# Performance work log

Measured on AMD Instinct MI355X. Metric: run time of the kernel, lower is better.

The kernel has to match this reference:

```python
import jax, jax.numpy as jnp
import numpy as np

DIM = 256
HID = 128


def setup_inputs() -> dict:
    key = jax.random.key(0)
    ks = jax.random.split(key, 10)
    B, T = 8, 2048
    s_in = 1.0 / np.sqrt(DIM)
    s_h = 1.0 / np.sqrt(HID)
    return {
        "x": jax.random.normal(ks[0], (B, T, DIM), jnp.float32),
        "adapt_bias": jax.random.normal(ks[1], (B, T, T), jnp.float32),
        "Wq": jax.random.uniform(ks[2], (HID, DIM), jnp.float32, -s_in, s_in),
        "bq": jax.random.uniform(ks[3], (HID,), jnp.float32, -s_in, s_in),
        "Wk": jax.random.uniform(ks[4], (HID, DIM), jnp.float32, -s_in, s_in),
        "bk": jax.random.uniform(ks[5], (HID,), jnp.float32, -s_in, s_in),
        "Wv": jax.random.uniform(ks[6], (HID, DIM), jnp.float32, -s_in, s_in),
        "bv": jax.random.uniform(ks[7], (HID,), jnp.float32, -s_in, s_in),
        "Wp": jax.random.uniform(ks[8], (DIM, HID), jnp.float32, -s_h, s_h),
        "bp": jax.random.uniform(ks[9], (DIM,), jnp.float32, -s_h, s_h),
    }


def reference(x, adapt_bias, Wq, bq, Wk, bk, Wv, bv, Wp, bp):
    # y = x (default). Q,K,V: [B,T,H]
    Q = jnp.einsum('btd,hd->bth', x, Wq) + bq
    K = jnp.einsum('btd,hd->bth', x, Wk) + bk
    V = jnp.einsum('btd,hd->bth', x, Wv) + bv
    Q_sig = jax.nn.sigmoid(Q)
    ab = jax.nn.softmax(adapt_bias, axis=-1)        # [B,T,T]
    Ksm = jax.nn.softmax(K, axis=1)                 # softmax over time dim
    eab = jnp.exp(ab)                               # [B,T,T]
    eK = jnp.exp(Ksm)                               # [B,T,H]
    num = jnp.einsum('bts,bsh->bth', eab, eK * V)
    den = jnp.einsum('bts,bsh->bth', eab, eK)
    Yt = Q_sig * (num / den)                        # [B,T,H]
    return jnp.einsum('bth,dh->btd', Yt, Wp) + bp   # [B,T,DIM]
```

## Files before the change

### kernel.cpp

```cpp
#include <hip/hip_runtime.h>
#include <hip/hip_bf16.h>

#define B_ 8
#define T_ 2048
#define D_ 256
#define H_ 128

typedef float f32x4 __attribute__((ext_vector_type(4)));
typedef short bf16x8 __attribute__((ext_vector_type(8)));

__device__ __forceinline__ unsigned short f2bf(float f){
  union { float f; unsigned u; } v; v.f = f;
  unsigned u = v.u;
  unsigned r = (u + 0x7FFFu + ((u >> 16) & 1u)) >> 16;
  return (unsigned short)r;
}

#define GLL16(g, l) __builtin_amdgcn_global_load_lds( \
    (const __attribute__((address_space(1))) void*)(g), \
    (__attribute__((address_space(3))) void*)(l), 16, 0, 0)

__device__ __forceinline__ float blk_reduce(float v, bool is_max, float* sbuf){
  for(int o = 32; o > 0; o >>= 1){
    float t = __shfl_xor(v, o);
    v = is_max ? fmaxf(v, t) : (v + t);
  }
  int w = threadIdx.x >> 6;
  __syncthreads();
  if((threadIdx.x & 63) == 0) sbuf[w] = v;
  __syncthreads();
  float r = sbuf[0];
  for(int i = 1; i < 4; i++) r = is_max ? fmaxf(r, sbuf[i]) : (r + sbuf[i]);
  return r;
}

__global__ __launch_bounds__(256) void qkv_kernel(
    const float* __restrict__ x,
    const float* __restrict__ Wq, const float* __restrict__ bq,
    const float* __restrict__ Wk, const float* __restrict__ bk,
    const float* __restrict__ Wv, const float* __restrict__ bv,
    float* __restrict__ Qsig, float* __restrict__ Kt, float* __restrict__ Vt)
{
  const int mat = blockIdx.y;
  const int g0  = blockIdx.x * 64;
  const int tid = threadIdx.x;
  const float* W   = (mat == 0) ? Wq : (mat == 1) ? Wk : Wv;
  const float* bia = (mat == 0) ? bq : (mat == 1) ? bk : bv;

  __shared__ __align__(16) short As[64 * 32];
  __shared__ __align__(16) short Ws[128 * 32];
  __shared__ float tbuf[64][129];

  const int w = tid >> 6, lane = tid & 63, rl = lane & 15, kg = lane >> 4;
  f32x4 acc[8];
  for(int i = 0; i < 8; i++) acc[i] = (f32x4){0.f, 0.f, 0.f, 0.f};

  const int c = tid & 31, r8 = tid >> 5;
  for(int kk = 0; kk < 256; kk += 32){
    __syncthreads();
    for(int p = 0; p < 8; p++){
      int rr = r8 + p * 8;
      As[rr * 32 + c] = (short)f2bf(x[(size_t)(g0 + rr) * 256 + kk + c]);
    }
    for(int p = 0; p < 16; p++){
      int hh = r8 + p * 8;
      Ws[hh * 32 + c] = (short)f2bf(W[(size_t)hh * 256 + kk + c]);
    }
    __syncthreads();
    bf16x8 a = *(const bf16x8*)&As[(w * 16 + rl) * 32 + kg * 8];
    for(int cf = 0; cf < 8; cf++){
      bf16x8 bb = *(const bf16x8*)&Ws[(cf * 16 + rl) * 32 + kg * 8];
      acc[cf] = __builtin_amdgcn_mfma_f32_16x16x32_bf16(a, bb, acc[cf], 0, 0, 0);
    }
  }

  const int b = g0 >> 11, t0 = g0 & 2047;
  if(mat == 0){
    for(int cf = 0; cf < 8; cf++){
      int h = cf * 16 + rl;
      float bh = bia[h];
      for(int r = 0; r < 4; r++){
        int tl = w * 16 + kg * 4 + r;
        float v = acc[cf][r] + bh;
        Qsig[(size_t)(g0 + tl) * 128 + h] = 1.f / (1.f + __expf(-v));
      }
    }
  } else {
    for(int cf = 0; cf < 8; cf++){
      int h = cf * 16 + rl;
      float bh = bia[h];
      for(int r = 0; r < 4; r++){
        int tl = w * 16 + kg * 4 + r;
        tbuf[tl][h] = acc[cf][r] + bh;
      }
    }
    __syncthreads();
    float* dst = (mat == 1) ? Kt : Vt;
    int h = tid >> 1, part = tid & 1;
    float* drow = dst + (size_t)(b * 128 + h) * 2048 + t0 + part * 32;
    for(int i = 0; i < 32; i += 4){
      float4 o;
      o.x = tbuf[part * 32 + i + 0][h];
      o.y = tbuf[part * 32 + i + 1][h];
      o.z = tbuf[part * 32 + i + 2][h];
      o.w = tbuf[part * 32 + i + 3][h];
      *(float4*)(drow + i) = o;
    }
  }
}

__global__ __launch_bounds__(256) void colsm_kernel(
    const float* __restrict__ Kt, const float* __restrict__ Vt,
    unsigned short* __restrict__ Mt)
{
  __shared__ float sbuf[4];
  const int b  = blockIdx.x >> 5;
  const int hg = blockIdx.x & 31;
  const int tid = threadIdx.x;
  for(int i = 0; i < 4; i++){
    int h = hg * 4 + i;
    const float* kr = Kt + (size_t)(b * 128 + h) * 2048;
    const float* vr = Vt + (size_t)(b * 128 + h) * 2048;
    float4 k0 = *(const float4*)(kr + tid * 4);
    float4 k1 = *(const float4*)(kr + tid * 4 + 1024);
    float m = fmaxf(fmaxf(fmaxf(k0.x, k0.y), fmaxf(k0.z, k0.w)),
                    fmaxf(fmaxf(k1.x, k1.y), fmaxf(k1.z, k1.w)));
    m = blk_reduce(m, true, sbuf);
    float s = __expf(k0.x - m) + __expf(k0.y - m) + __expf(k0.z - m) + __expf(k0.w - m)
            + __expf(k1.x - m) + __expf(k1.y - m) + __expf(k1.z - m) + __expf(k1.w - m);
    s = blk_reduce(s, false, sbuf);
    float iz = 1.f / s;
    float4 v0 = *(const float4*)(vr + tid * 4);
    float4 v1 = *(const float4*)(vr + tid * 4 + 1024);
    unsigned short* ekvp = Mt + (size_t)(b * 256 + h) * 2048;
    unsigned short* ekp  = Mt + (size_t)(b * 256 + 128 + h) * 2048;
    ushort4 pv, pe;
    float e;
    e = __expf(__expf(k0.x - m) * iz); pv.x = f2bf(e * v0.x); pe.x = f2bf(e);
    e = __expf(__expf(k0.y - m) * iz); pv.y = f2bf(e * v0.y); pe.y = f2bf(e);
    e = __expf(__expf(k0.z - m) * iz); pv.z = f2bf(e * v0.z); pe.z = f2bf(e);
    e = __expf(__expf(k0.w - m) * iz); pv.w = f2bf(e * v0.w); pe.w = f2bf(e);
    ((ushort4*)ekvp)[tid] = pv;
    ((ushort4*)ekp)[tid]  = pe;
    e = __expf(__expf(k1.x - m) * iz); pv.x = f2bf(e * v1.x); pe.x = f2bf(e);
    e = __expf(__expf(k1.y - m) * iz); pv.y = f2bf(e * v1.y); pe.y = f2bf(e);
    e = __expf(__expf(k1.z - m) * iz); pv.z = f2bf(e * v1.z); pe.z = f2bf(e);
    e = __expf(__expf(k1.w - m) * iz); pv.w = f2bf(e * v1.w); pe.w = f2bf(e);
    ((ushort4*)ekvp)[tid + 256] = pv;
    ((ushort4*)ekp)[tid + 256]  = pe;
  }
}

__global__ __launch_bounds__(256) void softexp_kernel(
    const float* __restrict__ ab, unsigned short* __restrict__ eab)
{
  __shared__ float sbuf[4];
  const size_t row = blockIdx.x;
  const float* r = ab + row * 2048;
  const int tid = threadIdx.x;
  float4 v0 = *(const float4*)(r + tid * 4);
  float4 v1 = *(const float4*)(r + tid * 4 + 1024);
  float m = fmaxf(fmaxf(fmaxf(v0.x, v0.y), fmaxf(v0.z, v0.w)),
                  fmaxf(fmaxf(v1.x, v1.y), fmaxf(v1.z, v1.w)));
  m = blk_reduce(m, true, sbuf);
  float e0x = __expf(v0.x - m), e0y = __expf(v0.y - m);
  float e0z = __expf(v0.z - m), e0w = __expf(v0.w - m);
  float e1x = __expf(v1.x - m), e1y = __expf(v1.y - m);
  float e1z = __expf(v1.z - m), e1w = __expf(v1.w - m);
  float s = e0x + e0y + e0z + e0w + e1x + e1y + e1z + e1w;
  s = blk_reduce(s, false, sbuf);
  float iz = 1.f / s;
  ushort4 o;
  o.x = f2bf(__expf(e0x * iz)); o.y = f2bf(__expf(e0y * iz));
  o.z = f2bf(__expf(e0z * iz)); o.w = f2bf(__expf(e0w * iz));
  *(ushort4*)(eab + row * 2048 + tid * 4) = o;
  o.x = f2bf(__expf(e1x * iz)); o.y = f2bf(__expf(e1y * iz));
  o.z = f2bf(__expf(e1z * iz)); o.w = f2bf(__expf(e1w * iz));
  *(ushort4*)(eab + row * 2048 + tid * 4 + 1024) = o;
}

__global__ __launch_bounds__(256) void aft_gemm4(
    const unsigned short* __restrict__ eab,
    const unsigned short* __restrict__ Mt,
    const float* __restrict__ Qsig,
    unsigned short* __restrict__ Yt)
{
  __shared__ __align__(16) unsigned short As2[2][64 * 64];
  __shared__ __align__(16) unsigned short Bs2[2][128 * 64];

  const int bid = blockIdx.x;
  const int b   = bid & 7;
  const int idx = bid >> 3;
  const int rt  = idx >> 1;
  const int hb  = idx & 1;
  const int t0  = rt * 64;
  const int h0  = hb * 64;

  const int tid = threadIdx.x;
  const int w = tid >> 6, lane = tid & 63;
  const int rl = lane & 15, kg = lane >> 4;
  const int wr = w >> 1, wc = w & 1;

  const int lr = lane >> 3;
  const int cc = (lane & 7) ^ lr;

  const size_t rowbase = (size_t)b * 2048 + t0;
  const unsigned short* a_src = eab + (rowbase + (size_t)(w * 16 + lr)) * 2048 + cc * 8;
  const int mtrow = (w < 2) ? (h0 + w * 32 + lr) : (128 + h0 + (w - 2) * 32 + lr);
  const unsigned short* b_src = Mt + ((size_t)b * 256 + mtrow) * 2048 + cc * 8;

  f32x4 acc[2][4];
#pragma unroll
  for(int i = 0; i < 2; i++)
#pragma unroll
    for(int j = 0; j < 4; j++) acc[i][j] = (f32x4){0.f, 0.f, 0.f, 0.f};

  auto stage = [&](int buf, int t){
#pragma unroll
    for(int i = 0; i < 2; i++)
      GLL16(a_src + (size_t)i * 8 * 2048 + t * 64, &As2[buf][(w * 16 + i * 8) * 64]);
#pragma unroll
    for(int i = 0; i < 4; i++)
      GLL16(b_src + (size_t)i * 8 * 2048 + t * 64, &Bs2[buf][(w * 32 + i * 8) * 64]);
  };

  const int rx = rl & 7;
  stage(0, 0);
  stage(1, 1);

  for(int t = 0; t < 32; ++t){
    const int cur = t & 1;
    if(t < 31) asm volatile("s_waitcnt vmcnt(6)" ::: "memory");
    else       asm volatile("s_waitcnt vmcnt(0)" ::: "memory");
    __builtin_amdgcn_s_barrier();
    asm volatile("" ::: "memory");

    bf16x8 af[2][2], bf[2][4];
#pragma unroll
    for(int ks = 0; ks < 2; ++ks){
      const int slot = ((ks * 4 + kg) ^ rx) * 8;
      af[ks][0] = *(const bf16x8*)&As2[cur][(wr * 32 + rl) * 64 + slot];
      af[ks][1] = *(const bf16x8*)&As2[cur][(wr * 32 + 16 + rl) * 64 + slot];
#pragma unroll
      for(int cf = 0; cf < 4; ++cf){
        const int brow = ((cf < 2) ? (wc * 32 + cf * 16)
                                   : (64 + wc * 32 + (cf - 2) * 16)) + rl;
        bf[ks][cf] = *(const bf16x8*)&Bs2[cur][brow * 64 + slot];
      }
    }
    asm volatile("s_waitcnt lgkmcnt(0)" ::: "memory");
    __builtin_amdgcn_sched_barrier(0);
    __builtin_amdgcn_s_barrier();
    asm volatile("" ::: "memory");

    if(t < 30) stage(cur, t + 2);

    __builtin_amdgcn_s_setprio(1);
#pragma unroll
    for(int ks = 0; ks < 2; ++ks)
#pragma unroll
      for(int cf = 0; cf < 4; ++cf){
        acc[0][cf] = __builtin_amdgcn_mfma_f32_16x16x32_bf16(af[ks][0], bf[ks][cf], acc[0][cf], 0, 0, 0);
        acc[1][cf] = __builtin_amdgcn_mfma_f32_16x16x32_bf16(af[ks][1], bf[ks][cf], acc[1][cf], 0, 0, 0);
      }
    __builtin_amdgcn_s_setprio(0);
  }

#pragma unroll
  for(int rf = 0; rf < 2; ++rf)
#pragma unroll
    for(int cf = 0; cf < 2; ++cf){
      const int h = h0 + wc * 32 + cf * 16 + rl;
#pragma unroll
      for(int r = 0; r < 4; ++r){
        const int tl = wr * 32 + rf * 16 + kg * 4 + r;
        const size_t g = rowbase + tl;
        float num = acc[rf][cf][r], den = acc[rf][cf + 2][r];
        float q = Qsig[g * 128 + h];
        Yt[g * 128 + h] = f2bf(q * num / den);
      }
    }
}

__global__ __launch_bounds__(256) void outproj_kernel(
    const unsigned short* __restrict__ Yt, const float* __restrict__ Wp,
    const float* __restrict__ bp, float* __restrict__ out)
{
  __shared__ __align__(16) short As[64 * 32];
  __shared__ __align__(16) short Bs[256 * 32];
  const int g0 = blockIdx.x * 64;
  const int tid = threadIdx.x;
  const int w = tid >> 6, lane = tid & 63, rl = lane & 15, kg = lane >> 4;
  f32x4 acc[16];
  for(int i = 0; i < 16; i++) acc[i] = (f32x4){0.f, 0.f, 0.f, 0.f};

  const int ar = tid >> 2, apart = tid & 3;
  const int c = tid & 31, dr = tid >> 5;
  for(int k = 0; k < 128; k += 32){
    __syncthreads();
    *(uint4*)&As[ar * 32 + apart * 8] =
        *(const uint4*)(Yt + (size_t)(g0 + ar) * 128 + k + apart * 8);
    for(int p = 0; p < 32; p++){
      int d = dr + p * 8;
      Bs[d * 32 + c] = (short)f2bf(Wp[(size_t)d * 128 + k + c]);
    }
    __syncthreads();
    bf16x8 a = *(const bf16x8*)&As[(w * 16 + rl) * 32 + kg * 8];
    for(int cf = 0; cf < 16; cf++){
      bf16x8 bb = *(const bf16x8*)&Bs[(cf * 16 + rl) * 32 + kg * 8];
      acc[cf] = __builtin_amdgcn_mfma_f32_16x16x32_bf16(a, bb, acc[cf], 0, 0, 0);
    }
  }
  for(int cf = 0; cf < 16; cf++){
    int d = cf * 16 + rl;
    float bpd = bp[d];
    for(int r = 0; r < 4; r++){
      int tl = w * 16 + kg * 4 + r;
      out[(size_t)(g0 + tl) * 256 + d] = acc[cf][r] + bpd;
    }
  }
}

extern "C" void kernel_launch(void* const* d_in, const int* in_sizes, int n_in,
                              void* d_out, int out_size, void* d_ws, size_t ws_size,
                              hipStream_t stream)
{
  const float* x  = (const float*)d_in[0];
  const float* ab = (const float*)d_in[1];
  const float* Wq = (const float*)d_in[2];
  const float* bq = (const float*)d_in[3];
  const float* Wk = (const float*)d_in[4];
  const float* bk = (const float*)d_in[5];
  const float* Wv = (const float*)d_in[6];
  const float* bv = (const float*)d_in[7];
  const float* Wp = (const float*)d_in[8];
  const float* bp = (const float*)d_in[9];
  float* out = (float*)d_out;

  char* ws = (char*)d_ws;
  float* Qsig          = (float*)(ws);
  float* Kt            = (float*)(ws + 8388608);
  float* Vt            = (float*)(ws + 16777216);
  unsigned short* Mt   = (unsigned short*)(ws + 25165824);
  unsigned short* eab  = (unsigned short*)(ws + 33554432);
  unsigned short* Yt   = (unsigned short*)(ws + 8388608);

  qkv_kernel<<<dim3(256, 3), 256, 0, stream>>>(x, Wq, bq, Wk, bk, Wv, bv, Qsig, Kt, Vt);
  colsm_kernel<<<256, 256, 0, stream>>>(Kt, Vt, Mt);
  softexp_kernel<<<16384, 256, 0, stream>>>(ab, eab);
  aft_gemm4<<<512, 256, 0, stream>>>(eab, Mt, Qsig, Yt);
  outproj_kernel<<<256, 256, 0, stream>>>(Yt, Wp, bp, out);
}
```

Baseline: 96.51 us.

## Enlarge AFT GEMM tile to 128 rows with triple-buffered LDS, single barrier

The main AFT GEMM block tile grows from 64 to 128 time rows, so each loaded Mt tile is reused across twice as many rows and the grid halves to 256 blocks. The LDS pipeline moves from double to triple buffering, which drops the second barrier per k-step, issues the prefetch right after the first barrier, and interleaves LDS reads with MFMAs. The cost is more LDS and accumulator registers per block and fewer blocks, which may lower occupancy and leave some of the 256 CUs with less overlap.

```diff
diff --git a/kernel.cpp b/kernel.cpp
--- a/kernel.cpp
+++ b/kernel.cpp
@@ -179,21 +179,21 @@
   *(ushort4*)(eab + row * 2048 + tid * 4 + 1024) = o;
 }
 
-__global__ __launch_bounds__(256) void aft_gemm4(
+__global__ __launch_bounds__(256) void aft_gemm5(
     const unsigned short* __restrict__ eab,
     const unsigned short* __restrict__ Mt,
     const float* __restrict__ Qsig,
     unsigned short* __restrict__ Yt)
 {
-  __shared__ __align__(16) unsigned short As2[2][64 * 64];
-  __shared__ __align__(16) unsigned short Bs2[2][128 * 64];
+  __shared__ __align__(16) unsigned short As2[3][128 * 64];
+  __shared__ __align__(16) unsigned short Bs2[3][128 * 64];
 
   const int bid = blockIdx.x;
   const int b   = bid & 7;
   const int idx = bid >> 3;
   const int rt  = idx >> 1;
   const int hb  = idx & 1;
-  const int t0  = rt * 64;
+  const int t0  = rt * 128;
   const int h0  = hb * 64;
 
   const int tid = threadIdx.x;
@@ -201,24 +201,24 @@
   const int rl = lane & 15, kg = lane >> 4;
   const int wr = w >> 1, wc = w & 1;
 
-  const int lr = lane >> 3;
-  const int cc = (lane & 7) ^ lr;
+  const int lr8 = lane >> 3;
+  const int cc  = (lane & 7) ^ lr8;
 
   const size_t rowbase = (size_t)b * 2048 + t0;
-  const unsigned short* a_src = eab + (rowbase + (size_t)(w * 16 + lr)) * 2048 + cc * 8;
-  const int mtrow = (w < 2) ? (h0 + w * 32 + lr) : (128 + h0 + (w - 2) * 32 + lr);
+  const unsigned short* a_src = eab + (rowbase + (size_t)(w * 32 + lr8)) * 2048 + cc * 8;
+  const int mtrow = (w < 2) ? (h0 + w * 32 + lr8) : (128 + h0 + (w - 2) * 32 + lr8);
   const unsigned short* b_src = Mt + ((size_t)b * 256 + mtrow) * 2048 + cc * 8;
 
-  f32x4 acc[2][4];
-#pragma unroll
-  for(int i = 0; i < 2; i++)
+  f32x4 acc[4][4];
+#pragma unroll
+  for(int i = 0; i < 4; i++)
 #pragma unroll
     for(int j = 0; j < 4; j++) acc[i][j] = (f32x4){0.f, 0.f, 0.f, 0.f};
 
   auto stage = [&](int buf, int t){
 #pragma unroll
-    for(int i = 0; i < 2; i++)
-      GLL16(a_src + (size_t)i * 8 * 2048 + t * 64, &As2[buf][(w * 16 + i * 8) * 64]);
+    for(int i = 0; i < 4; i++)
+      GLL16(a_src + (size_t)i * 8 * 2048 + t * 64, &As2[buf][(w * 32 + i * 8) * 64]);
 #pragma unroll
     for(int i = 0; i < 4; i++)
       GLL16(b_src + (size_t)i * 8 * 2048 + t * 64, &Bs2[buf][(w * 32 + i * 8) * 64]);
@@ -228,54 +228,49 @@
   stage(0, 0);
   stage(1, 1);
 
+  int cur = 0;
   for(int t = 0; t < 32; ++t){
-    const int cur = t & 1;
-    if(t < 31) asm volatile("s_waitcnt vmcnt(6)" ::: "memory");
+    if(t < 31) asm volatile("s_waitcnt vmcnt(8)" ::: "memory");
     else       asm volatile("s_waitcnt vmcnt(0)" ::: "memory");
     __builtin_amdgcn_s_barrier();
-    asm volatile("" ::: "memory");
-
-    bf16x8 af[2][2], bf[2][4];
+    if(t < 30){
+      int nb = cur + 2; if(nb >= 3) nb -= 3;
+      stage(nb, t + 2);
+    }
 #pragma unroll
     for(int ks = 0; ks < 2; ++ks){
       const int slot = ((ks * 4 + kg) ^ rx) * 8;
-      af[ks][0] = *(const bf16x8*)&As2[cur][(wr * 32 + rl) * 64 + slot];
-      af[ks][1] = *(const bf16x8*)&As2[cur][(wr * 32 + 16 + rl) * 64 + slot];
-#pragma unroll
-      for(int cf = 0; cf < 4; ++cf){
+      bf16x8 a[4], bb[4];
+#pragma unroll
+      for(int m = 0; m < 4; m++)
+        a[m] = *(const bf16x8*)&As2[cur][(wr * 64 + m * 16 + rl) * 64 + slot];
+#pragma unroll
+      for(int cf = 0; cf < 4; cf++){
         const int brow = ((cf < 2) ? (wc * 32 + cf * 16)
                                    : (64 + wc * 32 + (cf - 2) * 16)) + rl;
-        bf[ks][cf] = *(const bf16x8*)&Bs2[cur][brow * 64 + slot];
+        bb[cf] = *(const bf16x8*)&Bs2[cur][brow * 64 + slot];
       }
+#pragma unroll
+      for(int m = 0; m < 4; m++)
+#pragma unroll
+        for(int cf = 0; cf < 4; cf++)
+          acc[m][cf] = __builtin_amdgcn_mfma_f32_16x16x32_bf16(a[m], bb[cf], acc[m][cf], 0, 0, 0);
     }
     asm volatile("s_waitcnt lgkmcnt(0)" ::: "memory");
     __builtin_amdgcn_sched_barrier(0);
-    __builtin_amdgcn_s_barrier();
-    asm volatile("" ::: "memory");
-
-    if(t < 30) stage(cur, t + 2);
-
-    __builtin_amdgcn_s_setprio(1);
-#pragma unroll
-    for(int ks = 0; ks < 2; ++ks)
-#pragma unroll
-      for(int cf = 0; cf < 4; ++cf){
-        acc[0][cf] = __builtin_amdgcn_mfma_f32_16x16x32_bf16(af[ks][0], bf[ks][cf], acc[0][cf], 0, 0, 0);
-        acc[1][cf] = __builtin_amdgcn_mfma_f32_16x16x32_bf16(af[ks][1], bf[ks][cf], acc[1][cf], 0, 0, 0);
-      }
-    __builtin_amdgcn_s_setprio(0);
-  }
-
-#pragma unroll
-  for(int rf = 0; rf < 2; ++rf)
+    cur += 1; if(cur >= 3) cur -= 3;
+  }
+
+#pragma unroll
+  for(int m = 0; m < 4; ++m)
 #pragma unroll
     for(int cf = 0; cf < 2; ++cf){
       const int h = h0 + wc * 32 + cf * 16 + rl;
 #pragma unroll
       for(int r = 0; r < 4; ++r){
-        const int tl = wr * 32 + rf * 16 + kg * 4 + r;
+        const int tl = wr * 64 + m * 16 + kg * 4 + r;
         const size_t g = rowbase + tl;
-        float num = acc[rf][cf][r], den = acc[rf][cf + 2][r];
+        float num = acc[m][cf][r], den = acc[m][cf + 2][r];
         float q = Qsig[g * 128 + h];
         Yt[g * 128 + h] = f2bf(q * num / den);
       }
@@ -348,6 +343,6 @@
   qkv_kernel<<<dim3(256, 3), 256, 0, stream>>>(x, Wq, bq, Wk, bk, Wv, bv, Qsig, Kt, Vt);
   colsm_kernel<<<256, 256, 0, stream>>>(Kt, Vt, Mt);
   softexp_kernel<<<16384, 256, 0, stream>>>(ab, eab);
-  aft_gemm4<<<512, 256, 0, stream>>>(eab, Mt, Qsig, Yt);
+  aft_gemm5<<<256, 256, 0, stream>>>(eab, Mt, Qsig, Yt);
   outproj_kernel<<<256, 256, 0, stream>>>(Yt, Wp, bp, out);
 }
```

Result: slower. 112.6 us (+16.7%).
